# Performance work log

Hardware: AMD Instinct MI355X
Metric: run time of the kernel (lower is better)

The kernel has to match this reference:

```python
import jax, jax.numpy as jnp
import numpy as np

BETA = 0.25
CODEBOOK_SIZE = 1024
EMB_DIM = 256


def setup_inputs() -> dict:
    key = jax.random.key(0)
    k1, k2 = jax.random.split(key)
    z = jax.random.normal(k1, (32, EMB_DIM, 32, 32), dtype=jnp.float32)  # NCHW
    # torch init: uniform(-1/K, 1/K)
    lim = 1.0 / CODEBOOK_SIZE
    codebook = jax.random.uniform(k2, (CODEBOOK_SIZE, EMB_DIM), dtype=jnp.float32,
                                  minval=-lim, maxval=lim)
    return {"z": z, "codebook": codebook}


def reference(z, codebook):
    # z: [B, C, H, W] -> [B, H, W, C]
    zp = jnp.transpose(z, (0, 2, 3, 1))
    B, H, W, D = zp.shape
    zf = zp.reshape(-1, D)  # [N, D]
    K = codebook.shape[0]

    # pairwise squared distances: ||z||^2 + ||e||^2 - 2 z e^T  -> [N, K]
    d = ((zf * zf).sum(axis=1, keepdims=True)
         + (codebook * codebook).sum(axis=1)
         - 2.0 * jnp.einsum('nd,kd->nk', zf, codebook))
    mean_distance = jnp.mean(d)

    idx = jnp.argmin(d, axis=1)  # [N]
    # direct gather instead of one-hot matmul (same math)
    z_q = codebook[idx].reshape(B, H, W, D)

    loss = (BETA * jnp.mean((jax.lax.stop_gradient(z_q) - zp) ** 2)
            + jnp.mean((z_q - jax.lax.stop_gradient(zp)) ** 2))

    # straight-through estimator
    z_q_st = zp + jax.lax.stop_gradient(z_q - zp)

    # perplexity from mean one-hot usage (bincount via scatter-add)
    N = zf.shape[0]
    counts = jnp.zeros((K,), dtype=zf.dtype).at[idx].add(1.0)
    e_mean = counts / N
    perplexity = jnp.exp(-jnp.sum(e_mean * jnp.log(e_mean + 1e-10)))

    z_q_out = jnp.transpose(z_q_st, (0, 3, 1, 2))  # back to NCHW
    return z_q_out, loss, perplexity, idx, mean_distance
```

## Files before the change

kernel.cpp:

```cpp
#include <hip/hip_runtime.h>
#include <hip/hip_bf16.h>


#define NPTS   32768
#define KCODE  1024
#define DDIM   256
#define HWSZ   1024
#define ZSTRB  262144
#define ZELEMS 8388608

#define OUT_LOSS 8388608
#define OUT_PERP 8388609
#define OUT_IDX  8388610
#define OUT_MD   8421378

#define WS_IDX     0
#define WS_COUNTS  131072
#define WS_RLIST   135168
#define WS_RCOUNT  266240
#define WS_LOSSSUM 266248
#define WS_ZSQ     266256
#define WS_ENSUM   266264
#define WS_CHSUM   266272
#define WS_ESUM    268320
#define WS_ENORM   270368
#define WS_CBT     274464
#define WS_CBHI    1323040
#define WS_CBLO    1847328

#define MARGIN 3e-4f

#define RTILE 8

typedef short  s16x8 __attribute__((ext_vector_type(8)));
typedef unsigned short u16x8 __attribute__((ext_vector_type(8)));
typedef float  f32x4 __attribute__((ext_vector_type(4)));

__device__ __forceinline__ unsigned short bf16_rne(float f) {
    unsigned int u = __float_as_uint(f);
    return (unsigned short)((u + 0x7FFFu + ((u >> 16) & 1u)) >> 16);
}

__global__ __launch_bounds__(256) void init_kernel(char* ws) {
    int t = threadIdx.x;
    int* counts = (int*)(ws + WS_COUNTS);
    for (int i = t; i < 1024; i += 256) counts[i] = 0;
    if (t == 0) *(int*)(ws + WS_RCOUNT) = 0;
    double* dbl = (double*)(ws + WS_LOSSSUM);
    for (int i = t; i < 515; i += 256) dbl[i] = 0.0;
}

__device__ __forceinline__ float np_sumsq256(const float* p) {
    float tot[2];
    #pragma unroll
    for (int h = 0; h < 2; ++h) {
        const float* a = p + h * 128;
        float r[8];
        #pragma unroll
        for (int j = 0; j < 8; ++j) { float v = a[j]; float s = v * v; asm volatile("" : "+v"(s)); r[j] = s; }
        for (int i = 8; i < 128; i += 8) {
            #pragma unroll
            for (int j = 0; j < 8; ++j) { float v = a[i + j]; float s = v * v; asm volatile("" : "+v"(s)); r[j] += s; }
        }
        tot[h] = ((r[0] + r[1]) + (r[2] + r[3])) + ((r[4] + r[5]) + (r[6] + r[7]));
    }
    return tot[0] + tot[1];
}

__global__ __launch_bounds__(256) void prep2_kernel(const float* __restrict__ cb,
                                                    float* __restrict__ enorm,
                                                    float* __restrict__ cbT,
                                                    unsigned short* __restrict__ cbhi,
                                                    unsigned short* __restrict__ cblo,
                                                    double* __restrict__ esum,
                                                    double* __restrict__ enormsum) {
    __shared__ float tile[16][257];
    int t = threadIdx.x;
    int k0 = blockIdx.x * 16;

    #pragma unroll
    for (int i = 0; i < 4; ++i) {
        int f = t + 256 * i;
        int r = f >> 6;
        int c4 = (f & 63) << 2;
        float4 v = *(const float4*)(cb + (size_t)(k0 + r) * DDIM + c4);
        tile[r][c4] = v.x; tile[r][c4 + 1] = v.y; tile[r][c4 + 2] = v.z; tile[r][c4 + 3] = v.w;
    }
    __syncthreads();

    if (t < 16) {
        float s = np_sumsq256(&tile[t][0]);
        enorm[k0 + t] = s;
        double en = (double)s;
        for (int o = 8; o; o >>= 1) en += __shfl_down(en, o, 64);
        if (t == 0) atomicAdd(enormsum, en);
    }

    double cs = 0.0;
    for (int r = 0; r < 16; ++r) cs += (double)tile[r][t];
    atomicAdd(&esum[t], cs);

    {
        int kloc = t & 15, dg = t >> 4;
        #pragma unroll
        for (int dd = 0; dd < 16; ++dd) {
            int d = dd * 16 + dg;
            cbT[(size_t)d * KCODE + k0 + kloc] = tile[kloc][d];
        }
    }

    {
        int row = t >> 4;
        int d0 = (t & 15) * 16;
        #pragma unroll
        for (int j = 0; j < 2; ++j) {
            u16x8 H, L;
            #pragma unroll
            for (int e = 0; e < 8; ++e) {
                float f = tile[row][d0 + j * 8 + e];
                unsigned short h = bf16_rne(f);
                H[e] = h;
                L[e] = bf16_rne(f - __uint_as_float((unsigned int)h << 16));
            }
            *(u16x8*)(cbhi + (size_t)(k0 + row) * DDIM + d0 + j * 8) = H;
            *(u16x8*)(cblo + (size_t)(k0 + row) * DDIM + d0 + j * 8) = L;
        }
    }
}

__global__ __launch_bounds__(256, 4) void screen_kernel(const float* __restrict__ z,
                                                        const unsigned short* __restrict__ cbhi,
                                                        const unsigned short* __restrict__ cblo,
                                                        const float* __restrict__ enorm,
                                                        int* __restrict__ ws_idx,
                                                        int* __restrict__ rlist,
                                                        int* __restrict__ rcount) {
    int tid = threadIdx.x;
    int n0 = blockIdx.x * 64;
    int b = n0 >> 10, hw0 = n0 & 1023;
    int lane = tid & 63;
    int w = tid >> 6;
    int col = lane & 15;
    int kq = lane >> 4;

    const float* zp = z + (size_t)b * ZSTRB + (hw0 + w * 16 + col);
    s16x8 ah[8];
    #pragma unroll
    for (int kc = 0; kc < 8; ++kc) {
        u16x8 H;
        #pragma unroll
        for (int e = 0; e < 8; ++e)
            H[e] = bf16_rne(zp[(size_t)(kc * 32 + kq * 8 + e) << 10]);
        union { u16x8 u; s16x8 s; } cvt; cvt.u = H;
        ah[kc] = cvt.s;
    }

    float best[4] = {3.4e38f, 3.4e38f, 3.4e38f, 3.4e38f};
    float sec[4]  = {3.4e38f, 3.4e38f, 3.4e38f, 3.4e38f};
    int bidx[4] = {0, 0, 0, 0};

    const char* bhbase = (const char*)cbhi + col * 512 + kq * 16;
    const char* blbase = (const char*)cblo + col * 512 + kq * 16;

    #pragma unroll 1
    for (int chunk = 0; chunk < 64; ++chunk) {
        const char* bh = bhbase + chunk * 8192;
        const char* bl = blbase + chunk * 8192;
        f32x4 hh = {0.f, 0.f, 0.f, 0.f};
        f32x4 hl = {0.f, 0.f, 0.f, 0.f};
        #pragma unroll
        for (int kc = 0; kc < 8; ++kc) {
            s16x8 vbh = *(const s16x8*)(bh + kc * 64);
            s16x8 vbl = *(const s16x8*)(bl + kc * 64);
            hh = __builtin_amdgcn_mfma_f32_16x16x32_bf16(ah[kc], vbh, hh, 0, 0, 0);
            hl = __builtin_amdgcn_mfma_f32_16x16x32_bf16(ah[kc], vbl, hl, 0, 0, 0);
        }
        int k = chunk * 16 + col;
        float ek = enorm[k];
        #pragma unroll
        for (int r = 0; r < 4; ++r) {
            float dot = hh[r] + hl[r];
            float c = fmaf(-2.f, dot, ek);
            if (c < best[r]) { sec[r] = best[r]; best[r] = c; bidx[r] = k; }
            else if (c < sec[r]) sec[r] = c;
        }
    }

    #pragma unroll
    for (int m = 1; m < 16; m <<= 1) {
        #pragma unroll
        for (int r = 0; r < 4; ++r) {
            float ob = __shfl_xor(best[r], m, 64);
            float os = __shfl_xor(sec[r], m, 64);
            int   oi = __shfl_xor(bidx[r], m, 64);
            if (ob < best[r] || (ob == best[r] && oi < bidx[r])) {
                sec[r] = fminf(best[r], os);
                best[r] = ob; bidx[r] = oi;
            } else {
                sec[r] = fminf(sec[r], ob);
            }
        }
    }

    if (col == 0) {
        #pragma unroll
        for (int r = 0; r < 4; ++r) {
            int n = n0 + w * 16 + kq * 4 + r;
            ws_idx[n] = bidx[r];
            if (sec[r] - best[r] < MARGIN) {
                int slot = atomicAdd(rcount, 1);
                if (slot < NPTS) rlist[slot] = n;
            }
        }
    }
}

__global__ __launch_bounds__(256) void recheck_kernel(const float* __restrict__ z,
                                                      const float* __restrict__ cbT,
                                                      const float* __restrict__ enorm,
                                                      int* __restrict__ ws_idx,
                                                      const int* __restrict__ rlist,
                                                      const int* __restrict__ rcount) {
    __shared__ float zs[RTILE][DDIM + 1];
    __shared__ float s8[RTILE];
    __shared__ int   nn[RTILE];
    __shared__ float bv[256];
    __shared__ int   bi[256];
    int t = threadIdx.x;
    int cnt = *rcount; if (cnt > NPTS) cnt = NPTS;
    int ntiles = (cnt + RTILE - 1) / RTILE;

    for (int tile = blockIdx.x; tile < ntiles; tile += gridDim.x) {
        #pragma unroll
        for (int p = 0; p < RTILE; ++p) {
            int i = tile * RTILE + p;
            int real = (i < cnt);
            int n = rlist[real ? i : (cnt - 1)];
            if (t == 0) nn[p] = real ? n : -1;
            int b = n >> 10, hw = n & 1023;
            zs[p][t] = z[(size_t)b * ZSTRB + (size_t)t * HWSZ + hw];
        }
        __syncthreads();
        if (t < RTILE) s8[t] = np_sumsq256(&zs[t][0]);
        __syncthreads();

        float bestv[RTILE]; int besti[RTILE];
        #pragma unroll
        for (int p = 0; p < RTILE; ++p) { bestv[p] = 3.4e38f; besti[p] = 0; }

        #pragma unroll 1
        for (int j = 0; j < 4; ++j) {
            int k = t + 256 * j;
            double acc[RTILE];
            #pragma unroll
            for (int p = 0; p < RTILE; ++p) acc[p] = 0.0;
            const float* cp = cbT + k;
            #pragma unroll 2
            for (int d = 0; d < DDIM; ++d) {
                double c = (double)cp[d * KCODE];
                #pragma unroll
                for (int p = 0; p < RTILE; ++p)
                    acc[p] = fma(c, (double)zs[p][d], acc[p]);
            }
            float ek = enorm[k];
            #pragma unroll
            for (int p = 0; p < RTILE; ++p) {
                float E = (float)acc[p];
                float w = 2.0f * E;
                float u = s8[p] + ek;
                float dd = u - w;
                if (dd < bestv[p]) { bestv[p] = dd; besti[p] = k; }
            }
        }

        for (int p = 0; p < RTILE; ++p) {
            bv[t] = bestv[p]; bi[t] = besti[p];
            __syncthreads();
            for (int s2 = 128; s2; s2 >>= 1) {
                if (t < s2) {
                    if (bv[t + s2] < bv[t] || (bv[t + s2] == bv[t] && bi[t + s2] < bi[t])) {
                        bv[t] = bv[t + s2]; bi[t] = bi[t + s2];
                    }
                }
                __syncthreads();
            }
            if (t == 0 && nn[p] >= 0) ws_idx[nn[p]] = bi[0];
            __syncthreads();
        }
    }
}

__global__ __launch_bounds__(256) void hist_kernel(const int* __restrict__ ws_idx,
                                                   int* __restrict__ counts,
                                                   float* __restrict__ out_idx) {
    __shared__ int h[KCODE];
    int t = threadIdx.x;
    for (int i = t; i < KCODE; i += 256) h[i] = 0;
    __syncthreads();
    int n = blockIdx.x * 256 + t;
    int idx = ws_idx[n];
    out_idx[n] = (float)idx;
    atomicAdd(&h[idx], 1);
    __syncthreads();
    for (int i = t; i < KCODE; i += 256) { int c = h[i]; if (c) atomicAdd(&counts[i], c); }
}

__global__ __launch_bounds__(256) void out_kernel(const float* __restrict__ z,
                                                  const float* __restrict__ cb,
                                                  const int* __restrict__ ws_idx,
                                                  float* __restrict__ out,
                                                  double* __restrict__ lossSum,
                                                  double* __restrict__ chsum,
                                                  double* __restrict__ zsq) {
    int t = threadIdx.x;
    size_t base = (size_t)blockIdx.x * 1024;
    int c = blockIdx.x & 255;
    int b = blockIdx.x >> 8;
    int hw = t * 4;
    const float4 zv = *(const float4*)(z + base + hw);
    int4 iv = *(const int4*)(ws_idx + b * HWSZ + hw);
    float q0 = cb[(size_t)iv.x * DDIM + c];
    float q1 = cb[(size_t)iv.y * DDIM + c];
    float q2 = cb[(size_t)iv.z * DDIM + c];
    float q3 = cb[(size_t)iv.w * DDIM + c];
    float t0 = q0 - zv.x, t1 = q1 - zv.y, t2 = q2 - zv.z, t3 = q3 - zv.w;
    float4 o; o.x = zv.x + t0; o.y = zv.y + t1; o.z = zv.z + t2; o.w = zv.w + t3;
    *(float4*)(out + base + hw) = o;

    double ls  = (double)t0 * t0 + (double)t1 * t1 + (double)t2 * t2 + (double)t3 * t3;
    double zs  = (double)zv.x + (double)zv.y + (double)zv.z + (double)zv.w;
    double zq2 = (double)zv.x * zv.x + (double)zv.y * zv.y + (double)zv.z * zv.z + (double)zv.w * zv.w;

    __shared__ double r1[4], r2[4], r3[4];
    for (int o2 = 32; o2; o2 >>= 1) {
        ls  += __shfl_down(ls,  o2, 64);
        zs  += __shfl_down(zs,  o2, 64);
        zq2 += __shfl_down(zq2, o2, 64);
    }
    if ((t & 63) == 0) { int w = t >> 6; r1[w] = ls; r2[w] = zs; r3[w] = zq2; }
    __syncthreads();
    if (t == 0) {
        atomicAdd(lossSum, r1[0] + r1[1] + r1[2] + r1[3]);
        atomicAdd(&chsum[c], r2[0] + r2[1] + r2[2] + r2[3]);
        atomicAdd(zsq, r3[0] + r3[1] + r3[2] + r3[3]);
    }
}

__global__ __launch_bounds__(256) void fin_kernel(const int* __restrict__ counts,
                                                  const double* __restrict__ lossSum,
                                                  const double* __restrict__ chsum,
                                                  const double* __restrict__ esum,
                                                  const double* __restrict__ zsq,
                                                  const double* __restrict__ enormsum,
                                                  float* __restrict__ out) {
    int t = threadIdx.x;
    double ent = 0.0;
    for (int i = t; i < KCODE; i += 256) {
        float em = (float)counts[i] / 32768.0f;
        ent += (double)(em * logf(em + 1e-10f));
    }
    double pd = chsum[t] * esum[t];

    __shared__ double r1[4], r2[4];
    for (int o2 = 32; o2; o2 >>= 1) {
        ent += __shfl_down(ent, o2, 64);
        pd  += __shfl_down(pd,  o2, 64);
    }
    if ((t & 63) == 0) { int w = t >> 6; r1[w] = ent; r2[w] = pd; }
    __syncthreads();
    if (t == 0) {
        double ENT = r1[0] + r1[1] + r1[2] + r1[3];
        double PD  = r2[0] + r2[1] + r2[2] + r2[3];
        float m = (float)(*lossSum / (double)ZELEMS);
        out[OUT_LOSS] = 0.25f * m + m;
        out[OUT_PERP] = expf((float)(-ENT));
        double md = *zsq / (double)NPTS + *enormsum / (double)KCODE
                    - (2.0 / ((double)NPTS * (double)KCODE)) * PD;
        out[OUT_MD] = (float)md;
    }
}

extern "C" void kernel_launch(void* const* d_in, const int* in_sizes, int n_in,
                              void* d_out, int out_size, void* d_ws, size_t ws_size,
                              hipStream_t stream) {
    const float* z  = (const float*)d_in[0];
    const float* cb = (const float*)d_in[1];
    float* out = (float*)d_out;
    char* ws = (char*)d_ws;

    int*    ws_idx   = (int*)(ws + WS_IDX);
    int*    counts   = (int*)(ws + WS_COUNTS);
    int*    rlist    = (int*)(ws + WS_RLIST);
    int*    rcount   = (int*)(ws + WS_RCOUNT);
    double* lossSum  = (double*)(ws + WS_LOSSSUM);
    double* zsq      = (double*)(ws + WS_ZSQ);
    double* enormsum = (double*)(ws + WS_ENSUM);
    double* chsum    = (double*)(ws + WS_CHSUM);
    double* esum     = (double*)(ws + WS_ESUM);
    float*  enorm    = (float*)(ws + WS_ENORM);
    float*  cbT      = (float*)(ws + WS_CBT);
    unsigned short* cbhi = (unsigned short*)(ws + WS_CBHI);
    unsigned short* cblo = (unsigned short*)(ws + WS_CBLO);

    hipLaunchKernelGGL(init_kernel, dim3(1), dim3(256), 0, stream, ws);
    hipLaunchKernelGGL(prep2_kernel, dim3(64), dim3(256), 0, stream,
                       cb, enorm, cbT, cbhi, cblo, esum, enormsum);
    hipLaunchKernelGGL(screen_kernel, dim3(512), dim3(256), 0, stream,
                       z, cbhi, cblo, enorm, ws_idx, rlist, rcount);
    hipLaunchKernelGGL(recheck_kernel, dim3(512), dim3(256), 0, stream,
                       z, cbT, enorm, ws_idx, rlist, rcount);
    hipLaunchKernelGGL(hist_kernel, dim3(128), dim3(256), 0, stream,
                       ws_idx, counts, out + OUT_IDX);
    hipLaunchKernelGGL(out_kernel, dim3(8192), dim3(256), 0, stream,
                       z, cb, ws_idx, out, lossSum, chsum, zsq);
    hipLaunchKernelGGL(fin_kernel, dim3(1), dim3(256), 0, stream,
                       counts, lossSum, chsum, esum, zsq, enormsum, out);
}
```

Before: 731.1 us.

## Split codebook screening across two grid halves and merge per-point top-2

The screen kernel now splits the codebook into two halves via a second grid dimension, doubling the number of blocks. Each half writes per-point best, second-best and index, and a new merge kernel combines them and builds the recheck list. The hi/lo bf16 split moves from the codebook to z, and the MFMA accumulation is spread over four independent accumulators to shorten dependency chains. The out kernel gathers from the transposed codebook for better coalescing, at the cost of an extra launch and workspace traffic for the partial results.

```diff
diff --git a/kernel.cpp b/kernel.cpp
--- a/kernel.cpp
+++ b/kernel.cpp
@@ -26,7 +26,9 @@
 #define WS_ENORM   270368
 #define WS_CBT     274464
 #define WS_CBHI    1323040
-#define WS_CBLO    1847328
+#define WS_COLB    1847328
+#define WS_COLS    2109472
+#define WS_COLI    2371616
 
 #define MARGIN 3e-4f
 
@@ -71,7 +73,6 @@
                                                     float* __restrict__ enorm,
                                                     float* __restrict__ cbT,
                                                     unsigned short* __restrict__ cbhi,
-                                                    unsigned short* __restrict__ cblo,
                                                     double* __restrict__ esum,
                                                     double* __restrict__ enormsum) {
     __shared__ float tile[16][257];
@@ -114,75 +115,71 @@
         int d0 = (t & 15) * 16;
         #pragma unroll
         for (int j = 0; j < 2; ++j) {
-            u16x8 H, L;
+            u16x8 H;
             #pragma unroll
-            for (int e = 0; e < 8; ++e) {
-                float f = tile[row][d0 + j * 8 + e];
-                unsigned short h = bf16_rne(f);
-                H[e] = h;
-                L[e] = bf16_rne(f - __uint_as_float((unsigned int)h << 16));
-            }
+            for (int e = 0; e < 8; ++e) H[e] = bf16_rne(tile[row][d0 + j * 8 + e]);
             *(u16x8*)(cbhi + (size_t)(k0 + row) * DDIM + d0 + j * 8) = H;
-            *(u16x8*)(cblo + (size_t)(k0 + row) * DDIM + d0 + j * 8) = L;
         }
     }
 }
 
 __global__ __launch_bounds__(256, 4) void screen_kernel(const float* __restrict__ z,
                                                         const unsigned short* __restrict__ cbhi,
-                                                        const unsigned short* __restrict__ cblo,
                                                         const float* __restrict__ enorm,
-                                                        int* __restrict__ ws_idx,
-                                                        int* __restrict__ rlist,
-                                                        int* __restrict__ rcount) {
+                                                        float* __restrict__ colb,
+                                                        float* __restrict__ colsec,
+                                                        int* __restrict__ coli) {
     int tid = threadIdx.x;
     int n0 = blockIdx.x * 64;
+    int kbase = blockIdx.y * 512;
     int b = n0 >> 10, hw0 = n0 & 1023;
     int lane = tid & 63;
     int w = tid >> 6;
-    int col = lane & 15;
+    int colslot = lane & 15;
     int kq = lane >> 4;
 
-    const float* zp = z + (size_t)b * ZSTRB + (hw0 + w * 16 + col);
-    s16x8 ah[8];
+    const float* zp = z + (size_t)b * ZSTRB + (hw0 + w * 16 + colslot);
+    s16x8 ah[8], al[8];
     #pragma unroll
     for (int kc = 0; kc < 8; ++kc) {
-        u16x8 H;
-        #pragma unroll
-        for (int e = 0; e < 8; ++e)
-            H[e] = bf16_rne(zp[(size_t)(kc * 32 + kq * 8 + e) << 10]);
-        union { u16x8 u; s16x8 s; } cvt; cvt.u = H;
-        ah[kc] = cvt.s;
+        u16x8 H, L;
+        #pragma unroll
+        for (int e = 0; e < 8; ++e) {
+            float f = zp[(size_t)(kc * 32 + kq * 8 + e) << 10];
+            unsigned short h = bf16_rne(f);
+            H[e] = h;
+            L[e] = bf16_rne(f - __uint_as_float((unsigned int)h << 16));
+        }
+        union { u16x8 u; s16x8 s; } c1, c2; c1.u = H; c2.u = L;
+        ah[kc] = c1.s; al[kc] = c2.s;
     }
 
     float best[4] = {3.4e38f, 3.4e38f, 3.4e38f, 3.4e38f};
     float sec[4]  = {3.4e38f, 3.4e38f, 3.4e38f, 3.4e38f};
     int bidx[4] = {0, 0, 0, 0};
 
-    const char* bhbase = (const char*)cbhi + col * 512 + kq * 16;
-    const char* blbase = (const char*)cblo + col * 512 + kq * 16;
-
-    #pragma unroll 1
-    for (int chunk = 0; chunk < 64; ++chunk) {
-        const char* bh = bhbase + chunk * 8192;
-        const char* bl = blbase + chunk * 8192;
-        f32x4 hh = {0.f, 0.f, 0.f, 0.f};
-        f32x4 hl = {0.f, 0.f, 0.f, 0.f};
+    const char* bhbase = (const char*)cbhi + (size_t)kbase * 512 + colslot * 512 + kq * 16;
+
+    #pragma unroll 2
+    for (int chunk = 0; chunk < 32; ++chunk) {
+        const char* bh = bhbase + (size_t)chunk * 8192;
+        f32x4 c[4];
+        #pragma unroll
+        for (int q = 0; q < 4; ++q) c[q] = (f32x4){0.f, 0.f, 0.f, 0.f};
         #pragma unroll
         for (int kc = 0; kc < 8; ++kc) {
             s16x8 vbh = *(const s16x8*)(bh + kc * 64);
-            s16x8 vbl = *(const s16x8*)(bl + kc * 64);
-            hh = __builtin_amdgcn_mfma_f32_16x16x32_bf16(ah[kc], vbh, hh, 0, 0, 0);
-            hl = __builtin_amdgcn_mfma_f32_16x16x32_bf16(ah[kc], vbl, hl, 0, 0, 0);
-        }
-        int k = chunk * 16 + col;
+            c[kc & 3] = __builtin_amdgcn_mfma_f32_16x16x32_bf16(ah[kc], vbh, c[kc & 3], 0, 0, 0);
+            c[kc & 3] = __builtin_amdgcn_mfma_f32_16x16x32_bf16(al[kc], vbh, c[kc & 3], 0, 0, 0);
+        }
+        int k = kbase + chunk * 16 + colslot;
         float ek = enorm[k];
         #pragma unroll
         for (int r = 0; r < 4; ++r) {
-            float dot = hh[r] + hl[r];
-            float c = fmaf(-2.f, dot, ek);
-            if (c < best[r]) { sec[r] = best[r]; best[r] = c; bidx[r] = k; }
-            else if (c < sec[r]) sec[r] = c;
+            float dot = (c[0][r] + c[1][r]) + (c[2][r] + c[3][r]);
+            float cr = fmaf(-2.f, dot, ek);
+            if (cr < best[r]) { sec[r] = best[r]; best[r] = cr; bidx[r] = k; }
+            else if (cr < sec[r]) sec[r] = cr;
         }
     }
 
@@ -202,16 +199,35 @@
         }
     }
 
-    if (col == 0) {
+    if (colslot == 0) {
+        int cbase = blockIdx.y * NPTS;
         #pragma unroll
         for (int r = 0; r < 4; ++r) {
             int n = n0 + w * 16 + kq * 4 + r;
-            ws_idx[n] = bidx[r];
-            if (sec[r] - best[r] < MARGIN) {
-                int slot = atomicAdd(rcount, 1);
-                if (slot < NPTS) rlist[slot] = n;
-            }
-        }
+            colb[cbase + n] = best[r];
+            colsec[cbase + n] = sec[r];
+            coli[cbase + n] = bidx[r];
+        }
+    }
+}
+
+__global__ __launch_bounds__(256) void merge_kernel(const float* __restrict__ colb,
+                                                    const float* __restrict__ colsec,
+                                                    const int* __restrict__ coli,
+                                                    int* __restrict__ ws_idx,
+                                                    int* __restrict__ rlist,
+                                                    int* __restrict__ rcount) {
+    int n = blockIdx.x * 256 + threadIdx.x;
+    float B = colb[n], S = colsec[n];
+    int I = coli[n];
+    float b2 = colb[NPTS + n], s2 = colsec[NPTS + n];
+    int i2 = coli[NPTS + n];
+    if (b2 < B) { S = fminf(B, s2); I = i2; B = b2; }
+    else        { S = fminf(S, b2); }
+    ws_idx[n] = I;
+    if (S - B < MARGIN) {
+        int slot = atomicAdd(rcount, 1);
+        if (slot < NPTS) rlist[slot] = n;
     }
 }
 
@@ -306,7 +322,7 @@
 }
 
 __global__ __launch_bounds__(256) void out_kernel(const float* __restrict__ z,
-                                                  const float* __restrict__ cb,
+                                                  const float* __restrict__ cbT,
                                                   const int* __restrict__ ws_idx,
                                                   float* __restrict__ out,
                                                   double* __restrict__ lossSum,
@@ -319,10 +335,11 @@
     int hw = t * 4;
     const float4 zv = *(const float4*)(z + base + hw);
     int4 iv = *(const int4*)(ws_idx + b * HWSZ + hw);
-    float q0 = cb[(size_t)iv.x * DDIM + c];
-    float q1 = cb[(size_t)iv.y * DDIM + c];
-    float q2 = cb[(size_t)iv.z * DDIM + c];
-    float q3 = cb[(size_t)iv.w * DDIM + c];
+    const float* crow = cbT + (size_t)c * KCODE;
+    float q0 = crow[iv.x];
+    float q1 = crow[iv.y];
+    float q2 = crow[iv.z];
+    float q3 = crow[iv.w];
     float t0 = q0 - zv.x, t1 = q1 - zv.y, t2 = q2 - zv.z, t3 = q3 - zv.w;
     float4 o; o.x = zv.x + t0; o.y = zv.y + t1; o.z = zv.z + t2; o.w = zv.w + t3;
     *(float4*)(out + base + hw) = o;
@@ -400,19 +417,23 @@
     float*  enorm    = (float*)(ws + WS_ENORM);
     float*  cbT      = (float*)(ws + WS_CBT);
     unsigned short* cbhi = (unsigned short*)(ws + WS_CBHI);
-    unsigned short* cblo = (unsigned short*)(ws + WS_CBLO);
+    float*  colb     = (float*)(ws + WS_COLB);
+    float*  colsec   = (float*)(ws + WS_COLS);
+    int*    coli     = (int*)(ws + WS_COLI);
 
     hipLaunchKernelGGL(init_kernel, dim3(1), dim3(256), 0, stream, ws);
     hipLaunchKernelGGL(prep2_kernel, dim3(64), dim3(256), 0, stream,
-                       cb, enorm, cbT, cbhi, cblo, esum, enormsum);
-    hipLaunchKernelGGL(screen_kernel, dim3(512), dim3(256), 0, stream,
-                       z, cbhi, cblo, enorm, ws_idx, rlist, rcount);
+                       cb, enorm, cbT, cbhi, esum, enormsum);
+    hipLaunchKernelGGL(screen_kernel, dim3(512, 2), dim3(256), 0, stream,
+                       z, cbhi, enorm, colb, colsec, coli);
+    hipLaunchKernelGGL(merge_kernel, dim3(128), dim3(256), 0, stream,
+                       colb, colsec, coli, ws_idx, rlist, rcount);
     hipLaunchKernelGGL(recheck_kernel, dim3(512), dim3(256), 0, stream,
                        z, cbT, enorm, ws_idx, rlist, rcount);
     hipLaunchKernelGGL(hist_kernel, dim3(128), dim3(256), 0, stream,
                        ws_idx, counts, out + OUT_IDX);
     hipLaunchKernelGGL(out_kernel, dim3(8192), dim3(256), 0, stream,
-                       z, cb, ws_idx, out, lossSum, chsum, zsq);
+                       z, cbT, ws_idx, out, lossSum, chsum, zsq);
     hipLaunchKernelGGL(fin_kernel, dim3(1), dim3(256), 0, stream,
                        counts, lossSum, chsum, esum, zsq, enormsum, out);
 }
```

After: 624.1 us. -14.6%, faster.
